# Optimization experiments

Measured on AMD Instinct MI355X. Metric: run time of the kernel, lower is better.

Reference implementation:

```python
import jax, jax.numpy as jnp
import numpy as np

BN_EPS = 1e-5

def setup_inputs() -> dict:
    key = jax.random.key(0)
    ks = jax.random.split(key, 11)
    B, C, H, W = 8, 256, 64, 64
    Ci = 128
    s_in = 1.0 / np.sqrt(C)   # kaiming-uniform-ish scale for 1x1 convs
    s_ci = 1.0 / np.sqrt(Ci)
    return {
        "x": jax.random.normal(ks[0], (B, C, H, W), dtype=jnp.float32),
        "g_w": jax.random.normal(ks[1], (Ci, C), dtype=jnp.float32) * s_in,
        "g_b": jax.random.normal(ks[2], (Ci,), dtype=jnp.float32) * s_in,
        "theta_w": jax.random.normal(ks[3], (Ci, C), dtype=jnp.float32) * s_in,
        "theta_b": jax.random.normal(ks[4], (Ci,), dtype=jnp.float32) * s_in,
        "phi_w": jax.random.normal(ks[5], (Ci, C), dtype=jnp.float32) * s_in,
        "phi_b": jax.random.normal(ks[6], (Ci,), dtype=jnp.float32) * s_in,
        "W_w": jax.random.normal(ks[7], (C, Ci), dtype=jnp.float32) * s_ci,
        "W_b": jax.random.normal(ks[8], (C,), dtype=jnp.float32) * s_ci,
        "bn_gamma": jax.random.uniform(ks[9], (C,), dtype=jnp.float32),
        "bn_beta": jax.random.normal(ks[10], (C,), dtype=jnp.float32) * 0.1,
    }

def _proj(w, b, xf):
    # 1x1 conv as channel GEMM: w [O,C], xf [B,C,N] -> [B,O,N]
    return jnp.einsum('oc,bcn->bon', w, xf) + b[None, :, None]

def reference(x, g_w, g_b, theta_w, theta_b, phi_w, phi_b, W_w, W_b, bn_gamma, bn_beta):
    B, C, H, W = x.shape
    N = H * W
    xf = x.reshape(B, C, N)
    g_x = _proj(g_w, g_b, xf).transpose(0, 2, 1)       # [B,N,Ci]
    theta_x = _proj(theta_w, theta_b, xf).transpose(0, 2, 1)  # [B,N,Ci]
    phi_x = _proj(phi_w, phi_b, xf)                     # [B,Ci,N]
    # unscaled single-head spatial attention
    f = jnp.einsum('bnc,bcm->bnm', theta_x, phi_x)      # [B,N,N]
    f_div_C = jax.nn.softmax(f, axis=-1)
    y = jnp.einsum('bnm,bmc->bnc', f_div_C, g_x)        # [B,N,Ci]
    y = y.transpose(0, 2, 1)                            # [B,Ci,N]
    Wy = _proj(W_w, W_b, y)                             # [B,C,N]
    # BatchNorm2d in training mode: stats over (B, N) per channel (biased var)
    mean = jnp.mean(Wy, axis=(0, 2), keepdims=True)
    var = jnp.mean((Wy - mean) ** 2, axis=(0, 2), keepdims=True)
    Wy_hat = (Wy - mean) * jax.lax.rsqrt(var + BN_EPS)
    Wy_bn = Wy_hat * bn_gamma[None, :, None] + bn_beta[None, :, None]
    z = Wy_bn.reshape(B, C, H, W) + x
    return z
```

## Files before the change

kernel.cpp:

```cpp
#include <hip/hip_runtime.h>
#include <cstddef>

#define NB 8
#define NC 256
#define NN 4096
#define NCI 128

typedef unsigned short ushort_t;
typedef __attribute__((ext_vector_type(8))) short bf16x8;
typedef __attribute__((ext_vector_type(4))) short bf16x4;
typedef __attribute__((ext_vector_type(4))) float f32x4;
typedef __attribute__((ext_vector_type(8))) unsigned short ushort8v;
typedef __attribute__((ext_vector_type(4))) unsigned short ushort4v;

__device__ __forceinline__ ushort_t f2bf(float f) {
  union { float f; unsigned int u; } x; x.f = f;
  unsigned int r = x.u + 0x7FFFu + ((x.u >> 16) & 1u);
  return (ushort_t)(r >> 16);
}
__device__ __forceinline__ float bf2f(ushort_t h) {
  union { unsigned int u; float f; } x; x.u = ((unsigned int)h) << 16;
  return x.f;
}
__device__ __forceinline__ void gld16(const void* g, void* l) {
  __builtin_amdgcn_global_load_lds(
      (const __attribute__((address_space(1))) unsigned int*)g,
      (__attribute__((address_space(3))) unsigned int*)l, 16, 0, 0);
}

__global__ __launch_bounds__(512) void conv_w_kernel(
    const float* __restrict__ th_w, const float* __restrict__ ph_w,
    const float* __restrict__ g_w,  const float* __restrict__ W_w,
    ushort_t* __restrict__ thw, ushort_t* __restrict__ thwl,
    ushort_t* __restrict__ phw, ushort_t* __restrict__ phwl,
    ushort_t* __restrict__ gw,  ushort_t* __restrict__ Wwf)
{
    const int t16 = blockIdx.x;
    const int p   = blockIdx.y;
    const int u = threadIdx.x >> 6, lane = threadIdx.x & 63;
    if (p < 3 && t16 >= 8) return;
    if (p == 3 && u >= 4) return;
    const float* w = (p == 0) ? th_w : (p == 1) ? ph_w : (p == 2) ? g_w : W_w;
    ushort_t* oh  = (p == 0) ? thw  : (p == 1) ? phw  : (p == 2) ? gw  : Wwf;
    ushort_t* ol  = (p == 0) ? thwl : (p == 1) ? phwl : nullptr;
    const int stride = (p == 3) ? NCI : NC;
    const int fr = t16 * 16 + (lane & 15);
    ushort8v hv, lv;
#pragma unroll
    for (int j = 0; j < 8; ++j) {
        int c = 32 * u + 8 * (lane >> 4) + j;
        float v = w[(size_t)fr * stride + c];
        ushort_t hi = f2bf(v);
        hv[j] = hi;
        lv[j] = f2bf(v - bf2f(hi));
    }
    size_t o = (p == 3) ? (((size_t)t16 * 4 + u) * 64 + lane) * 8
                        : (((size_t)t16 * 8 + u) * 64 + lane) * 8;
    *(ushort8v*)(oh + o) = hv;
    if (p < 2) *(ushort8v*)(ol + o) = lv;
}

__global__ __launch_bounds__(256, 2) void proj_mfma_kernel(
    const float* __restrict__ x,
    const ushort_t* __restrict__ thw, const ushort_t* __restrict__ thwl,
    const ushort_t* __restrict__ phw, const ushort_t* __restrict__ phwl,
    const ushort_t* __restrict__ gw,
    const float* __restrict__ th_b, const float* __restrict__ ph_b,
    const float* __restrict__ g_b,
    ushort_t* __restrict__ thh,
    ushort_t* __restrict__ phh, ushort_t* __restrict__ phl,
    ushort_t* __restrict__ gfr)
{
    const int tid = threadIdx.x;
    const int lane = tid & 63, wv = tid >> 6;
    const int b  = blockIdx.x >> 6;
    const int nt = (blockIdx.x & 63) * 4 + wv;
    const int h = lane >> 4, li = lane & 15;

    bf16x8 xh[8], xl[8];
#pragma unroll
    for (int u = 0; u < 8; ++u) {
#pragma unroll
        for (int j = 0; j < 8; ++j) {
            int c = 32 * u + 8 * h + j;
            float v = x[((size_t)b * NC + c) * NN + nt * 16 + li];
            ushort_t hi = f2bf(v);
            xh[u][j] = (short)hi;
            xl[u][j] = (short)f2bf(v - bf2f(hi));
        }
    }

#pragma unroll
    for (int u2 = 0; u2 < 4; ++u2) {
        f32x4 D0 = (f32x4){0.f,0.f,0.f,0.f}, D1 = (f32x4){0.f,0.f,0.f,0.f};
#pragma unroll
        for (int u = 0; u < 8; ++u) {
            bf16x8 a0h = *(const bf16x8*)(thw  + ((size_t)(2*u2)   * 8 + u) * 512 + lane * 8);
            bf16x8 a0l = *(const bf16x8*)(thwl + ((size_t)(2*u2)   * 8 + u) * 512 + lane * 8);
            bf16x8 a1h = *(const bf16x8*)(thw  + ((size_t)(2*u2+1) * 8 + u) * 512 + lane * 8);
            bf16x8 a1l = *(const bf16x8*)(thwl + ((size_t)(2*u2+1) * 8 + u) * 512 + lane * 8);
            D0 = __builtin_amdgcn_mfma_f32_16x16x32_bf16(a0h, xh[u], D0, 0, 0, 0);
            D0 = __builtin_amdgcn_mfma_f32_16x16x32_bf16(a0h, xl[u], D0, 0, 0, 0);
            D0 = __builtin_amdgcn_mfma_f32_16x16x32_bf16(a0l, xh[u], D0, 0, 0, 0);
            D1 = __builtin_amdgcn_mfma_f32_16x16x32_bf16(a1h, xh[u], D1, 0, 0, 0);
            D1 = __builtin_amdgcn_mfma_f32_16x16x32_bf16(a1h, xl[u], D1, 0, 0, 0);
            D1 = __builtin_amdgcn_mfma_f32_16x16x32_bf16(a1l, xh[u], D1, 0, 0, 0);
        }
        ushort8v hv;
#pragma unroll
        for (int r = 0; r < 4; ++r) hv[r]     = f2bf(D0[r] + th_b[u2 * 32 + 4 * h + r]);
#pragma unroll
        for (int r = 0; r < 4; ++r) hv[4 + r] = f2bf(D1[r] + th_b[u2 * 32 + 16 + 4 * h + r]);
        *(ushort8v*)(thh + (((size_t)b * 256 + nt) * 4 + u2) * 512 + lane * 8) = hv;
    }

    const int m32  = ((nt & 1) << 4) | li;
    const int mtp  = (m32 >> 2) & 1;
    const int rowp = ((m32 >> 3) << 2) | (m32 & 3);
#pragma unroll
    for (int u2 = 0; u2 < 4; ++u2) {
        f32x4 D0 = (f32x4){0.f,0.f,0.f,0.f}, D1 = (f32x4){0.f,0.f,0.f,0.f};
#pragma unroll
        for (int u = 0; u < 8; ++u) {
            bf16x8 a0h = *(const bf16x8*)(phw  + ((size_t)(2*u2)   * 8 + u) * 512 + lane * 8);
            bf16x8 a0l = *(const bf16x8*)(phwl + ((size_t)(2*u2)   * 8 + u) * 512 + lane * 8);
            bf16x8 a1h = *(const bf16x8*)(phw  + ((size_t)(2*u2+1) * 8 + u) * 512 + lane * 8);
            bf16x8 a1l = *(const bf16x8*)(phwl + ((size_t)(2*u2+1) * 8 + u) * 512 + lane * 8);
            D0 = __builtin_amdgcn_mfma_f32_16x16x32_bf16(a0h, xh[u], D0, 0, 0, 0);
            D0 = __builtin_amdgcn_mfma_f32_16x16x32_bf16(a0h, xl[u], D0, 0, 0, 0);
            D0 = __builtin_amdgcn_mfma_f32_16x16x32_bf16(a0l, xh[u], D0, 0, 0, 0);
            D1 = __builtin_amdgcn_mfma_f32_16x16x32_bf16(a1h, xh[u], D1, 0, 0, 0);
            D1 = __builtin_amdgcn_mfma_f32_16x16x32_bf16(a1h, xl[u], D1, 0, 0, 0);
            D1 = __builtin_amdgcn_mfma_f32_16x16x32_bf16(a1l, xh[u], D1, 0, 0, 0);
        }
        ushort8v hv, lv;
#pragma unroll
        for (int r = 0; r < 4; ++r) {
            float v = D0[r] + ph_b[u2 * 32 + 4 * h + r];
            ushort_t hi = f2bf(v);
            hv[r] = hi; lv[r] = f2bf(v - bf2f(hi));
        }
#pragma unroll
        for (int r = 0; r < 4; ++r) {
            float v = D1[r] + ph_b[u2 * 32 + 16 + 4 * h + r];
            ushort_t hi = f2bf(v);
            hv[4 + r] = hi; lv[4 + r] = f2bf(v - bf2f(hi));
        }
        size_t o = ((((size_t)b * 128 + (nt >> 1)) * 2 + mtp) * 4 + u2) * 512
                 + (size_t)(rowp + 16 * h) * 8;
        *(ushort8v*)(phh + o) = hv;
        *(ushort8v*)(phl + o) = lv;
    }

    const int h2 = (nt & 1) * 2 + (h >> 1);
    const int j0 = (h & 1) * 4;
#pragma unroll
    for (int cit = 0; cit < 8; ++cit) {
        f32x4 D = (f32x4){0.f,0.f,0.f,0.f};
#pragma unroll
        for (int u = 0; u < 8; ++u) {
            bf16x8 bv = *(const bf16x8*)(gw + ((size_t)cit * 8 + u) * 512 + lane * 8);
            D = __builtin_amdgcn_mfma_f32_16x16x32_bf16(xh[u], bv, D, 0, 0, 0);
        }
        float gb = g_b[cit * 16 + li];
        ushort4v pv;
#pragma unroll
        for (int r = 0; r < 4; ++r) pv[r] = f2bf(D[r] + gb);
        size_t o = (((size_t)b * 128 + (nt >> 1)) * 8 + cit) * 512
                 + (size_t)(li + 16 * h2) * 8 + j0;
        *(ushort4v*)(gfr + o) = pv;
    }
}

__global__ __launch_bounds__(256, 2) void attn_mfma_kernel(
    const ushort_t* __restrict__ thh,
    const ushort_t* __restrict__ phh, const ushort_t* __restrict__ phl,
    const ushort_t* __restrict__ gfr, float* __restrict__ pacc,
    float* __restrict__ pl)
{
    __shared__ __align__(16) char smem[49152];
    const int tid  = threadIdx.x;
    const int lane = tid & 63;
    const int wv   = tid >> 6;
    const int batch = blockIdx.x & 7;
    const int ih    = blockIdx.x >> 3;
    const int half  = ih & 1;
    const int qblk  = ih >> 1;
    const int qt0   = qblk * 8 + wv * 2;

    bf16x8 qh[2][4];
#pragma unroll
    for (int q = 0; q < 2; ++q)
#pragma unroll
        for (int u = 0; u < 4; ++u)
            qh[q][u] = *(const bf16x8*)(thh + (((size_t)batch * 256 + qt0 + q) * 4 + u) * 512 + (size_t)lane * 8);

    f32x4 accy[2][8];
#pragma unroll
    for (int q = 0; q < 2; ++q)
#pragma unroll
        for (int c = 0; c < 8; ++c) accy[q][c] = (f32x4){0.f, 0.f, 0.f, 0.f};
    float l_run[2] = {0.f, 0.f};

    const ushort_t* Kh = phh + (size_t)batch * 524288 + (size_t)half * 262144;
    const ushort_t* Kl = phl + (size_t)batch * 524288 + (size_t)half * 262144;
    const ushort_t* Vg = gfr + (size_t)batch * 524288 + (size_t)half * 262144;

    {
        size_t off = (size_t)tid * 8;
        gld16(Kh + off,        smem + tid * 16);
        gld16(Kh + off + 2048, smem + 4096  + tid * 16);
        gld16(Kl + off,        smem + 8192  + tid * 16);
        gld16(Kl + off + 2048, smem + 12288 + tid * 16);
        gld16(Vg + off,        smem + 16384 + tid * 16);
        gld16(Vg + off + 2048, smem + 20480 + tid * 16);
    }
    __syncthreads();

    for (int t = 0; t < 64; ++t) {
        const int cb = t & 1;
        if (t < 63) {
            size_t off = (size_t)(t + 1) * 4096 + (size_t)tid * 8;
            char* b2 = smem + (cb ^ 1) * 24576;
            gld16(Kh + off,        b2 + tid * 16);
            gld16(Kh + off + 2048, b2 + 4096  + tid * 16);
            gld16(Kl + off,        b2 + 8192  + tid * 16);
            gld16(Kl + off + 2048, b2 + 12288 + tid * 16);
            gld16(Vg + off,        b2 + 16384 + tid * 16);
            gld16(Vg + off + 2048, b2 + 20480 + tid * 16);
        }
        const char* buf = smem + cb * 24576;

        __builtin_amdgcn_s_setprio(1);
        f32x4 sA[2][2], sB[2][2];
#pragma unroll
        for (int q = 0; q < 2; ++q)
#pragma unroll
            for (int mt = 0; mt < 2; ++mt) {
                sA[q][mt] = (f32x4){0.f,0.f,0.f,0.f};
                sB[q][mt] = (f32x4){0.f,0.f,0.f,0.f};
            }
#pragma unroll
        for (int u = 0; u < 4; ++u) {
            bf16x8 kh0 = *(const bf16x8*)(buf + (0 * 4 + u) * 1024 + lane * 16);
            bf16x8 kh1 = *(const bf16x8*)(buf + (1 * 4 + u) * 1024 + lane * 16);
            bf16x8 kl0 = *(const bf16x8*)(buf + 8192 + (0 * 4 + u) * 1024 + lane * 16);
            bf16x8 kl1 = *(const bf16x8*)(buf + 8192 + (1 * 4 + u) * 1024 + lane * 16);
            sA[0][0] = __builtin_amdgcn_mfma_f32_16x16x32_bf16(kh0, qh[0][u], sA[0][0], 0, 0, 0);
            sA[1][0] = __builtin_amdgcn_mfma_f32_16x16x32_bf16(kh0, qh[1][u], sA[1][0], 0, 0, 0);
            sA[0][1] = __builtin_amdgcn_mfma_f32_16x16x32_bf16(kh1, qh[0][u], sA[0][1], 0, 0, 0);
            sA[1][1] = __builtin_amdgcn_mfma_f32_16x16x32_bf16(kh1, qh[1][u], sA[1][1], 0, 0, 0);
            sB[0][0] = __builtin_amdgcn_mfma_f32_16x16x32_bf16(kl0, qh[0][u], sB[0][0], 0, 0, 0);
            sB[1][0] = __builtin_amdgcn_mfma_f32_16x16x32_bf16(kl0, qh[1][u], sB[1][0], 0, 0, 0);
            sB[0][1] = __builtin_amdgcn_mfma_f32_16x16x32_bf16(kl1, qh[0][u], sB[0][1], 0, 0, 0);
            sB[1][1] = __builtin_amdgcn_mfma_f32_16x16x32_bf16(kl1, qh[1][u], sB[1][1], 0, 0, 0);
        }
        __builtin_amdgcn_s_setprio(0);

        bf16x8 pa[2];
#pragma unroll
        for (int q = 0; q < 2; ++q) {
            union { unsigned int w[4]; bf16x8 v; } pk;
            float lsum = 0.f;
#pragma unroll
            for (int mt = 0; mt < 2; ++mt) {
                f32x4 s = sA[q][mt] + sB[q][mt];
                float p0 = exp2f(fmaf(s[0], 1.4426950408889634f, -86.56170245333781f));
                float p1 = exp2f(fmaf(s[1], 1.4426950408889634f, -86.56170245333781f));
                float p2 = exp2f(fmaf(s[2], 1.4426950408889634f, -86.56170245333781f));
                float p3 = exp2f(fmaf(s[3], 1.4426950408889634f, -86.56170245333781f));
                lsum += (p0 + p1) + (p2 + p3);
                union { float f; unsigned int u; } b0, b1, b2, b3;
                b0.f = p0; b1.f = p1; b2.f = p2; b3.f = p3;
                pk.w[2 * mt]     = (b0.u >> 16) | (b1.u & 0xFFFF0000u);
                pk.w[2 * mt + 1] = (b2.u >> 16) | (b3.u & 0xFFFF0000u);
            }
            l_run[q] += lsum;
            pa[q] = pk.v;
        }

        __builtin_amdgcn_s_setprio(1);
#pragma unroll
        for (int cit = 0; cit < 8; ++cit) {
            bf16x8 vf = *(const bf16x8*)(buf + 16384 + cit * 1024 + lane * 16);
            accy[0][cit] = __builtin_amdgcn_mfma_f32_16x16x32_bf16(pa[0], vf, accy[0][cit], 0, 0, 0);
            accy[1][cit] = __builtin_amdgcn_mfma_f32_16x16x32_bf16(pa[1], vf, accy[1][cit], 0, 0, 0);
        }
        __builtin_amdgcn_s_setprio(0);
        __syncthreads();
    }

#pragma unroll
    for (int q = 0; q < 2; ++q) {
        l_run[q] += __shfl_xor(l_run[q], 16);
        l_run[q] += __shfl_xor(l_run[q], 32);
    }

    const int h = lane >> 4, li = lane & 15;
#pragma unroll
    for (int q = 0; q < 2; ++q) {
        float* pp = pacc + (size_t)half * 4194304
                  + ((size_t)batch * NN + (size_t)(qt0 + q) * 16) * NCI + li;
#pragma unroll
        for (int cit = 0; cit < 8; ++cit) {
            pp[(4 * h + 0) * NCI + cit * 16] = accy[q][cit][0];
            pp[(4 * h + 1) * NCI + cit * 16] = accy[q][cit][1];
            pp[(4 * h + 2) * NCI + cit * 16] = accy[q][cit][2];
            pp[(4 * h + 3) * NCI + cit * 16] = accy[q][cit][3];
        }
        if (lane < 16)
            pl[(((size_t)half * 8 + batch) * 256 + qt0 + q) * 16 + lane] = l_run[q];
    }
}

__global__ __launch_bounds__(256) void wy_kernel(
    const float* __restrict__ pacc, const float* __restrict__ pl,
    const ushort_t* __restrict__ Wwf, const float* __restrict__ W_b,
    float* __restrict__ Wy, float* __restrict__ bs, float* __restrict__ bs2)
{
    __shared__ ushort_t ys[8192];
    const int tid = threadIdx.x;
    const int lane = tid & 63, wv = tid >> 6;
    const int b = blockIdx.x >> 6;
    const int n0 = (blockIdx.x & 63) << 6;

    {
        const int nn = tid >> 2;
        const int q4 = tid & 3;
        const int n = n0 + nn;
        const int qt = n >> 4, qq = n & 15;
        float l0 = pl[((size_t)b * 256 + qt) * 16 + qq];
        float l1 = pl[((size_t)(8 + b) * 256 + qt) * 16 + qq];
        float inv = 1.0f / (l0 + l1);
        const float* p0 = pacc + ((size_t)b * NN + n) * NCI + q4 * 32;
        const float* p1 = p0 + 4194304;
#pragma unroll
        for (int gi = 0; gi < 4; ++gi) {
            float4 a0 = *(const float4*)(p0 + gi * 8);
            float4 a1 = *(const float4*)(p0 + gi * 8 + 4);
            float4 c0 = *(const float4*)(p1 + gi * 8);
            float4 c1 = *(const float4*)(p1 + gi * 8 + 4);
            ushort8v v;
            v[0] = f2bf((a0.x + c0.x) * inv);
            v[1] = f2bf((a0.y + c0.y) * inv);
            v[2] = f2bf((a0.z + c0.z) * inv);
            v[3] = f2bf((a0.w + c0.w) * inv);
            v[4] = f2bf((a1.x + c1.x) * inv);
            v[5] = f2bf((a1.y + c1.y) * inv);
            v[6] = f2bf((a1.z + c1.z) * inv);
            v[7] = f2bf((a1.w + c1.w) * inv);
            int sg = (q4 * 4 + gi) ^ (nn & 7);
            *(ushort8v*)(ys + nn * 128 + sg * 8) = v;
        }
    }
    __syncthreads();

    const int h = lane >> 4, li = lane & 15;
    bf16x8 wa[4][4];
#pragma unroll
    for (int ct = 0; ct < 4; ++ct)
#pragma unroll
        for (int kc = 0; kc < 4; ++kc)
            wa[ct][kc] = *(const bf16x8*)(Wwf + (((size_t)(wv * 4 + ct) * 4 + kc) * 64 + lane) * 8);
    float wb[4][4];
#pragma unroll
    for (int ct = 0; ct < 4; ++ct)
#pragma unroll
        for (int r = 0; r < 4; ++r)
            wb[ct][r] = W_b[wv * 64 + ct * 16 + 4 * h + r];

    float ps[4][4], ps2[4][4];
#pragma unroll
    for (int ct = 0; ct < 4; ++ct)
#pragma unroll
        for (int r = 0; r < 4; ++r) { ps[ct][r] = 0.f; ps2[ct][r] = 0.f; }

#pragma unroll
    for (int ct = 0; ct < 4; ++ct)
#pragma unroll
        for (int nt = 0; nt < 4; ++nt) {
            f32x4 D = (f32x4){0.f, 0.f, 0.f, 0.f};
            const int nn = nt * 16 + li;
#pragma unroll
            for (int kc = 0; kc < 4; ++kc) {
                int sg = (4 * kc + h) ^ (nn & 7);
                bf16x8 bv = *(const bf16x8*)(ys + nn * 128 + sg * 8);
                D = __builtin_amdgcn_mfma_f32_16x16x32_bf16(wa[ct][kc], bv, D, 0, 0, 0);
            }
            float* o = Wy + ((size_t)b * NC + wv * 64 + ct * 16 + 4 * h) * NN + n0 + nn;
#pragma unroll
            for (int r = 0; r < 4; ++r) {
                float v = D[r] + wb[ct][r];
                o[(size_t)r * NN] = v;
                ps[ct][r]  += v;
                ps2[ct][r] += v * v;
            }
        }

#pragma unroll
    for (int ct = 0; ct < 4; ++ct)
#pragma unroll
        for (int r = 0; r < 4; ++r) {
#pragma unroll
            for (int off = 1; off <= 8; off <<= 1) {
                ps[ct][r]  += __shfl_xor(ps[ct][r],  off);
                ps2[ct][r] += __shfl_xor(ps2[ct][r], off);
            }
        }
    if (li == 0) {
#pragma unroll
        for (int ct = 0; ct < 4; ++ct)
#pragma unroll
            for (int r = 0; r < 4; ++r) {
                int c = wv * 64 + ct * 16 + 4 * h + r;
                bs [(size_t)c * 512 + blockIdx.x] = ps[ct][r];
                bs2[(size_t)c * 512 + blockIdx.x] = ps2[ct][r];
            }
    }
}

__global__ __launch_bounds__(256) void bn_stats_kernel(
    const float* __restrict__ bs, const float* __restrict__ bs2,
    const float* __restrict__ gamma, const float* __restrict__ beta,
    float* __restrict__ scale, float* __restrict__ shift)
{
    const int c = blockIdx.x;
    const int tid = threadIdx.x;
    float s  = bs [(size_t)c * 512 + tid] + bs [(size_t)c * 512 + tid + 256];
    float s2 = bs2[(size_t)c * 512 + tid] + bs2[(size_t)c * 512 + tid + 256];
#pragma unroll
    for (int off = 1; off < 64; off <<= 1) {
        s  += __shfl_xor(s, off);
        s2 += __shfl_xor(s2, off);
    }
    __shared__ float red[8];
    const int wid = tid >> 6;
    if ((tid & 63) == 0) { red[wid] = s; red[4 + wid] = s2; }
    __syncthreads();
    if (tid == 0) {
        float S  = red[0] + red[1] + red[2] + red[3];
        float S2 = red[4] + red[5] + red[6] + red[7];
        const float invn = 1.f / (float)(NB * NN);
        float mean = S * invn;
        float var  = S2 * invn - mean * mean;
        float rstd = rsqrtf(var + 1e-5f);
        float sc = gamma[c] * rstd;
        scale[c] = sc;
        shift[c] = beta[c] - mean * sc;
    }
}

__global__ __launch_bounds__(256) void bn_apply_kernel(
    const float* __restrict__ Wy, const float* __restrict__ x,
    const float* __restrict__ scale, const float* __restrict__ shift,
    float* __restrict__ out)
{
    const size_t i4 = (size_t)blockIdx.x * 256 + threadIdx.x;
    const int c = (int)((i4 >> 10) & 255);
    float4 w  = ((const float4*)Wy)[i4];
    float4 xv = ((const float4*)x)[i4];
    const float sc = scale[c], sh = shift[c];
    float4 o;
    o.x = w.x * sc + sh + xv.x;
    o.y = w.y * sc + sh + xv.y;
    o.z = w.z * sc + sh + xv.z;
    o.w = w.w * sc + sh + xv.w;
    ((float4*)out)[i4] = o;
}

extern "C" void kernel_launch(void* const* d_in, const int* in_sizes, int n_in,
                              void* d_out, int out_size, void* d_ws, size_t ws_size,
                              hipStream_t stream) {
    const float* x     = (const float*)d_in[0];
    const float* g_w   = (const float*)d_in[1];
    const float* g_b   = (const float*)d_in[2];
    const float* th_w  = (const float*)d_in[3];
    const float* th_b  = (const float*)d_in[4];
    const float* ph_w  = (const float*)d_in[5];
    const float* ph_b  = (const float*)d_in[6];
    const float* W_w   = (const float*)d_in[7];
    const float* W_b   = (const float*)d_in[8];
    const float* gamma = (const float*)d_in[9];
    const float* beta  = (const float*)d_in[10];
    float* out = (float*)d_out;
    float* ws  = (float*)d_ws;

    ushort_t* thh = (ushort_t*)(ws);
    ushort_t* phh = (ushort_t*)(ws + 2097152);
    ushort_t* phl = (ushort_t*)(ws + 4194304);
    ushort_t* gfr = (ushort_t*)(ws + 6291456);
    float* Wy     = ws;
    float* pacc   = ws + 8388608;
    float* pl     = ws + 16777216;
    float* scale  = ws + 16842752;
    float* shift  = ws + 16843008;
    ushort_t* thw  = (ushort_t*)(ws + 16843264);
    ushort_t* phw  = (ushort_t*)(ws + 16859648);
    ushort_t* gw   = (ushort_t*)(ws + 16876032);
    ushort_t* Wwf  = (ushort_t*)(ws + 16892416);
    ushort_t* thwl = (ushort_t*)(ws + 16908800);
    ushort_t* phwl = (ushort_t*)(ws + 16925184);
    float* bs  = ws + 16941568;
    float* bs2 = ws + 17072640;

    conv_w_kernel<<<dim3(16, 4), 512, 0, stream>>>(
        th_w, ph_w, g_w, W_w, thw, thwl, phw, phwl, gw, Wwf);
    proj_mfma_kernel<<<512, 256, 0, stream>>>(
        x, thw, thwl, phw, phwl, gw, th_b, ph_b, g_b, thh, phh, phl, gfr);
    attn_mfma_kernel<<<512, 256, 0, stream>>>(thh, phh, phl, gfr, pacc, pl);
    wy_kernel<<<512, 256, 0, stream>>>(pacc, pl, Wwf, W_b, Wy, bs, bs2);
    bn_stats_kernel<<<256, 256, 0, stream>>>(bs, bs2, gamma, beta, scale, shift);
    bn_apply_kernel<<<8192, 256, 0, stream>>>(Wy, x, scale, shift, out);
}
```

Before: 201.2 us.

## Software-pipeline attention loop: defer PV MFMA by one tile with triple-buffered LDS

The attention loop moves from double to triple buffering in LDS. The P·V MFMAs for the previous key tile now run right after the current tile's QK MFMAs, inside one high-priority MFMA region. This aims to overlap the exp/softmax VALU work with matrix-core work and to fold two barriers per iteration into one (waitcnt plus s_barrier). In exchange, LDS per block grows to 72KB and a few extra registers stay live to hold the deferred probabilities, which may limit occupancy.

```diff
diff --git a/kernel.cpp b/kernel.cpp
--- a/kernel.cpp
+++ b/kernel.cpp
@@ -178,7 +178,7 @@
     const ushort_t* __restrict__ gfr, float* __restrict__ pacc,
     float* __restrict__ pl)
 {
-    __shared__ __align__(16) char smem[49152];
+    __shared__ __align__(16) char smem[73728];
     const int tid  = threadIdx.x;
     const int lane = tid & 63;
     const int wv   = tid >> 6;
@@ -201,6 +201,7 @@
 #pragma unroll
         for (int c = 0; c < 8; ++c) accy[q][c] = (f32x4){0.f, 0.f, 0.f, 0.f};
     float l_run[2] = {0.f, 0.f};
+    bf16x8 pa[2];
 
     const ushort_t* Kh = phh + (size_t)batch * 524288 + (size_t)half * 262144;
     const ushort_t* Kl = phl + (size_t)batch * 524288 + (size_t)half * 262144;
@@ -215,13 +216,19 @@
         gld16(Vg + off,        smem + 16384 + tid * 16);
         gld16(Vg + off + 2048, smem + 20480 + tid * 16);
     }
-    __syncthreads();
-
+
+    int cb = 0;
     for (int t = 0; t < 64; ++t) {
-        const int cb = t & 1;
+        asm volatile("s_waitcnt vmcnt(0)" ::: "memory");
+        __builtin_amdgcn_s_barrier();
+        __builtin_amdgcn_sched_barrier(0);
+
+        int nb = cb + 1; if (nb == 3) nb = 0;
+        int pb = cb + 2; if (pb == 3) { pb = 2; } else if (pb > 2) { pb -= 3; }
+        pb = cb + 2; if (pb >= 3) pb -= 3;
         if (t < 63) {
             size_t off = (size_t)(t + 1) * 4096 + (size_t)tid * 8;
-            char* b2 = smem + (cb ^ 1) * 24576;
+            char* b2 = smem + nb * 24576;
             gld16(Kh + off,        b2 + tid * 16);
             gld16(Kh + off + 2048, b2 + 4096  + tid * 16);
             gld16(Kl + off,        b2 + 8192  + tid * 16);
@@ -229,7 +236,8 @@
             gld16(Vg + off,        b2 + 16384 + tid * 16);
             gld16(Vg + off + 2048, b2 + 20480 + tid * 16);
         }
-        const char* buf = smem + cb * 24576;
+        const char* buf  = smem + cb * 24576;
+        const char* bufP = smem + pb * 24576;
 
         __builtin_amdgcn_s_setprio(1);
         f32x4 sA[2][2], sB[2][2];
@@ -255,9 +263,17 @@
             sB[0][1] = __builtin_amdgcn_mfma_f32_16x16x32_bf16(kl1, qh[0][u], sB[0][1], 0, 0, 0);
             sB[1][1] = __builtin_amdgcn_mfma_f32_16x16x32_bf16(kl1, qh[1][u], sB[1][1], 0, 0, 0);
         }
+
+        if (t > 0) {
+#pragma unroll
+            for (int cit = 0; cit < 8; ++cit) {
+                bf16x8 vf = *(const bf16x8*)(bufP + 16384 + cit * 1024 + lane * 16);
+                accy[0][cit] = __builtin_amdgcn_mfma_f32_16x16x32_bf16(pa[0], vf, accy[0][cit], 0, 0, 0);
+                accy[1][cit] = __builtin_amdgcn_mfma_f32_16x16x32_bf16(pa[1], vf, accy[1][cit], 0, 0, 0);
+            }
+        }
         __builtin_amdgcn_s_setprio(0);
 
-        bf16x8 pa[2];
 #pragma unroll
         for (int q = 0; q < 2; ++q) {
             union { unsigned int w[4]; bf16x8 v; } pk;
@@ -278,16 +294,18 @@
             l_run[q] += lsum;
             pa[q] = pk.v;
         }
-
-        __builtin_amdgcn_s_setprio(1);
+        __builtin_amdgcn_sched_barrier(0);
+        cb = nb;
+    }
+
+    {
+        const char* bufP = smem + 0 * 24576;
 #pragma unroll
         for (int cit = 0; cit < 8; ++cit) {
-            bf16x8 vf = *(const bf16x8*)(buf + 16384 + cit * 1024 + lane * 16);
+            bf16x8 vf = *(const bf16x8*)(bufP + 16384 + cit * 1024 + lane * 16);
             accy[0][cit] = __builtin_amdgcn_mfma_f32_16x16x32_bf16(pa[0], vf, accy[0][cit], 0, 0, 0);
             accy[1][cit] = __builtin_amdgcn_mfma_f32_16x16x32_bf16(pa[1], vf, accy[1][cit], 0, 0, 0);
         }
-        __builtin_amdgcn_s_setprio(0);
-        __syncthreads();
     }
 
 #pragma unroll
```

Result: faster. 192.6 us (-4.3%).
